# Optimization experiments

Measured on AMD Instinct MI355X. Metric: run time of the kernel, lower is better.

## Reference

```python
import jax, jax.numpy as jnp
import numpy as np

BLANK = 512            # blank_idx = vocab_size
DURATIONS = (1, 2, 3, 4)
SIGMA = 0.05           # logit under-normalization weight
NEG = -1e30            # safe -inf (keeps gradients finite)


def setup_inputs() -> dict:
    key = jax.random.key(0)
    k1, k2, k3 = jax.random.split(key, 3)
    B, T, U, V = 8, 256, 64, 512
    D = len(DURATIONS)
    label_acts = jax.random.normal(k1, (B, T, U + 1, V + 1), dtype=jnp.float32)
    duration_acts = jax.random.normal(k2, (B, T, U + 1, D), dtype=jnp.float32)
    targets = jax.random.randint(k3, (B, U), 0, V, dtype=jnp.int32)
    input_lengths = jnp.full((B,), T, dtype=jnp.int32)
    target_lengths = jnp.full((B,), U, dtype=jnp.int32)
    return {"label_acts": label_acts, "duration_acts": duration_acts,
            "targets": targets, "input_lengths": input_lengths,
            "target_lengths": target_lengths}


def _lag(x, d):
    # x: [T, ...] -> y with y[t] = x[t - d], NEG-padded at the front
    pad = jnp.full_like(x[:d], NEG)
    return jnp.concatenate([pad, x[: x.shape[0] - d]], axis=0)


def _tdt_loglike(label_acts, duration_acts, targets, input_lengths, target_lengths):
    B, T, U1, _ = label_acts.shape
    U = U1 - 1
    D = len(DURATIONS)

    lp = jax.nn.log_softmax(label_acts, axis=-1) - SIGMA        # [B,T,U+1,V+1]
    lpb = lp[..., BLANK]                                         # [B,T,U+1] blank logp
    lpy = jnp.take_along_axis(                                   # [B,T,U] target-label logp
        lp[:, :, :U, :], targets[:, None, :, None].astype(jnp.int32), axis=3
    )[..., 0]
    ld = jax.nn.log_softmax(duration_acts, axis=-1)              # [B,T,U+1,D]

    # time-major views for the scan
    lpb_t = jnp.transpose(lpb, (1, 0, 2))                        # [T,B,U+1]
    lpy_t = jnp.transpose(lpy, (1, 0, 2))                        # [T,B,U]
    ld_t = jnp.transpose(ld, (1, 0, 2, 3))                       # [T,B,U+1,D]

    # lagged emission terms: entry at scan step t is the value at t - duration
    lb_lag = jnp.stack([_lag(lpb_t, d) for d in DURATIONS], axis=1)                       # [T,D,B,U+1]
    ly_lag = jnp.stack([_lag(lpy_t, d) for d in DURATIONS], axis=1)                       # [T,D,B,U]
    ld_lag = jnp.stack([_lag(ld_t[..., i], d) for i, d in enumerate(DURATIONS)], axis=1)  # [T,D,B,U+1]

    dmax = max(DURATIONS)
    alpha0 = jnp.concatenate(
        [jnp.zeros((B, 1), jnp.float32), jnp.full((B, U), NEG, jnp.float32)], axis=1)     # [B,U+1]
    hist0 = jnp.concatenate(
        [alpha0[None], jnp.full((dmax - 1, B, U1), NEG, jnp.float32)], axis=0)            # [dmax,B,U+1]

    def step(hist, xs):
        # hist[a] = alpha[t-1-a]
        lb, ly, ldr = xs  # [D,B,U+1], [D,B,U], [D,B,U+1]
        blank_terms = jnp.stack([hist[d - 1] + lb[i] + ldr[i]
                                 for i, d in enumerate(DURATIONS)])      # [D,B,U+1]
        blank_in = jax.nn.logsumexp(blank_terms, axis=0)                 # [B,U+1]
        label_terms = jnp.stack([hist[d - 1][:, :U] + ly[i] + ldr[i][:, :U]
                                 for i, d in enumerate(DURATIONS)])      # [D,B,U]
        label_in = jax.nn.logsumexp(label_terms, axis=0)                 # [B,U]
        alpha_t = jnp.concatenate(
            [blank_in[:, :1], jnp.logaddexp(blank_in[:, 1:], label_in)], axis=1)
        hist = jnp.concatenate([alpha_t[None], hist[:-1]], axis=0)
        return hist, alpha_t

    _, alphas_rest = jax.lax.scan(step, hist0, (lb_lag[1:], ly_lag[1:], ld_lag[1:]))
    alphas = jnp.concatenate([alpha0[None], alphas_rest], axis=0)        # [T,B,U+1]

    # final: from (T_b - d, U_b) emit blank with duration d landing exactly at T_b
    dur = jnp.asarray(DURATIONS, jnp.int32)                              # [D]
    t_idx = input_lengths[:, None].astype(jnp.int32) - dur[None, :]      # [B,D]
    valid = t_idx >= 0
    t_safe = jnp.clip(t_idx, 0, T - 1)
    b_idx = jnp.arange(B)[:, None]
    u_idx = target_lengths[:, None].astype(jnp.int32)
    a_fin = alphas[t_safe, b_idx, u_idx]                                 # [B,D]
    lpb_fin = lpb[b_idx, t_safe, u_idx]                                  # [B,D]
    ld_fin = ld[b_idx, t_safe, u_idx, jnp.arange(D)[None, :]]            # [B,D]
    terms = jnp.where(valid, a_fin + lpb_fin + ld_fin, NEG)
    return jax.nn.logsumexp(terms, axis=1)                               # [B] log-likelihood


def reference(label_acts, duration_acts, targets, input_lengths, target_lengths):
    ll = _tdt_loglike(label_acts, duration_acts, targets, input_lengths, target_lengths)
    return jnp.mean(-ll)  # reduction='mean'
```

## Files before the change

### kernel.cpp

```cpp
#include <hip/hip_runtime.h>

#define TDT_B  8
#define TDT_T  256
#define TDT_U  64
#define TDT_U1 65
#define TDT_V1 513
#define TP     275
#define SIG    0.05f
#define SHIFT  3.0f

#define OFF_PYD 572000
#define OFF_GC  1135200

__global__ __launch_bounds__(256) void k_prep(
    const float* __restrict__ la, const float* __restrict__ da,
    const int* __restrict__ tgt, float* __restrict__ ws,
    float* __restrict__ out)
{
  if (blockIdx.x == 0 && threadIdx.x == 0) out[0] = 0.f;

  const int l = threadIdx.x & 63;
  const int r = (blockIdx.x << 2) + (threadIdx.x >> 6);
  const int u  = r % TDT_U1;
  const int bt = r / TDT_U1;
  const int t  = bt & (TDT_T - 1);
  const int b  = bt >> 8;

  const float* row = la + (size_t)r * TDT_V1;
  const int ofs = r & 1;
  const float2* p2 = (const float2*)(row + ofs);
  float2 w[4];
#pragma unroll
  for (int k = 0; k < 4; ++k) w[k] = p2[l + (k << 6)];
  const float extra = row[ofs ? 0 : 512];

  float m = extra;
#pragma unroll
  for (int k = 0; k < 4; ++k) m = fmaxf(m, fmaxf(w[k].x, w[k].y));
#pragma unroll
  for (int off = 32; off; off >>= 1) m = fmaxf(m, __shfl_xor(m, off));
  float s = (l == 0) ? __expf(extra - m) : 0.f;
#pragma unroll
  for (int k = 0; k < 4; ++k) s += __expf(w[k].x - m) + __expf(w[k].y - m);
#pragma unroll
  for (int off = 32; off; off >>= 1) s += __shfl_xor(s, off);
  const float lse = m + __logf(s);

  const float4 dv = *(const float4*)(da + ((size_t)r << 2));
  const float m4 = fmaxf(fmaxf(dv.x, dv.y), fmaxf(dv.z, dv.w));
  const float l4 = m4 + __logf(__expf(dv.x - m4) + __expf(dv.y - m4) +
                               __expf(dv.z - m4) + __expf(dv.w - m4));
  const float d0 = dv.x - l4 + SHIFT * 1.0f;
  const float d1 = dv.y - l4 + SHIFT * 2.0f;
  const float d2 = dv.z - l4 + SHIFT * 3.0f;
  const float d3 = dv.w - l4 + SHIFT * 4.0f;

  float4* WB4 = (float4*)ws;
  float4* WY4 = (float4*)(ws + OFF_PYD);
  float4* GC4 = (float4*)(ws + OFF_GC);

  const int tp = t + 4;
  const float xb = ofs ? w[3].y : extra;
  if (l == (ofs ? 63 : 0)) {
    const float pb = xb - lse - SIG;
    const float4 wb = make_float4(__expf(pb + d0), __expf(pb + d1),
                                  __expf(pb + d2), __expf(pb + d3));
    WB4[(b * TP + tp) * TDT_U1 + u] = wb;
    if (u == TDT_U) GC4[b * TP + tp] = wb;
  }

  const int tg = (u < TDT_U) ? tgt[b * TDT_U + u] : -1;
  bool own = false; float vt = 0.f;
#pragma unroll
  for (int k = 0; k < 4; ++k) {
    const int base = ofs + ((l + (k << 6)) << 1);
    if (base == tg)     { vt = w[k].x; own = true; }
    if (base + 1 == tg) { vt = w[k].y; own = true; }
  }
  if (ofs && tg == 0 && l == 0) { vt = extra; own = true; }
  if (own) {
    const float py = vt - lse - SIG;
    WY4[(b * TP + tp) * TDT_U + u] =
        make_float4(__expf(py + d0), __expf(py + d1), __expf(py + d2), __expf(py + d3));
  }

  if (t < 4 && l == 0) {
    const float4 z4 = make_float4(0.f, 0.f, 0.f, 0.f);
    WB4[(b * TP + t) * TDT_U1 + u] = z4;
    if (u == TDT_U) GC4[b * TP + t] = z4;
    if (u < TDT_U)  WY4[(b * TP + t) * TDT_U + u] = z4;
  }
}

__device__ __forceinline__ float shup1(float x) {
  const int r = __builtin_amdgcn_update_dpp(
      0, __float_as_int(x), 0x138, 0xf, 0xf, true);
  return __int_as_float(r);
}

__device__ __forceinline__ void gl2lds16(const float4* g, float4* lds) {
  __builtin_amdgcn_global_load_lds(
      (const __attribute__((address_space(1))) void*)g,
      (__attribute__((address_space(3))) void*)lds, 16, 0, 0);
}

__device__ __forceinline__ void fill_group(
    const float4* __restrict__ WB4p, const float4* __restrict__ WY4p,
    float4* ring, int j, int wv, int l)
{
  const int sb = 15 * j + wv;
  const int rb = 15 * (j % 3) + (wv - 1);
#pragma unroll
  for (int k = 0; k < 5; ++k) {
    const int s    = sb + 3 * k;
    const int slot = rb + 3 * k;
    gl2lds16(WB4p + (size_t)s * TDT_U1 + l, ring + slot * 128);
    gl2lds16(WY4p + (size_t)s * TDT_U  + l, ring + slot * 128 + 64);
  }
}

__global__ __launch_bounds__(256, 1) void k_dp(
    const float* __restrict__ ws, float* __restrict__ out)
{
  const int b  = blockIdx.x;
  const int wv = threadIdx.x >> 6;
  const int l  = threadIdx.x & 63;
  const float4* WB4p = (const float4*)ws + (size_t)b * (TP * TDT_U1);
  const float4* WY4p = (const float4*)(ws + OFF_PYD) + (size_t)b * (TP * TDT_U);
  const float4* GC4p = (const float4*)(ws + OFF_GC) + (size_t)b * TP;

  extern __shared__ float4 smem[];
  float4* ring = smem;
  float4* glds = smem + 45 * 128;

  if (wv != 0) {
    for (int i = (threadIdx.x - 64); i < TP; i += 192) glds[i] = GC4p[i];
    fill_group(WB4p, WY4p, ring, 0, wv, l);
    fill_group(WB4p, WY4p, ring, 1, wv, l);
  }
  __syncthreads();

  float4 B0,B1,B2,B3,B4,B5,B6,B7,B8,B9,B10,B11,B12,B13,B14;
  float4 Y0,Y1,Y2,Y3,Y4,Y5,Y6,Y7,Y8,Y9,Y10,Y11,Y12,Y13,Y14;
  float4 G0,G1,G2,G3,G4,G5,G6,G7,G8,G9,G10,G11,G12,G13,G14;
  float a1 = 0.f, a2 = 0.f, a3 = 0.f, a4 = 0.f;
  float c1 = 0.f, c2 = 0.f, c3 = 0.f, c4 = 0.f;
  float L = 0.f;

#define LOADSLOT(S, RS, TPI) do {            \
    const int _r = (RS) * 128;               \
    B##S = ring[_r + l];                     \
    Y##S = ring[_r + 64 + l];                \
    G##S = glds[TPI];                        \
  } while (0)

  if (wv == 0) {
    LOADSLOT(1, 0, 1);   LOADSLOT(2, 1, 2);   LOADSLOT(3, 2, 3);
    LOADSLOT(4, 3, 4);   LOADSLOT(5, 4, 5);   LOADSLOT(6, 5, 6);
    LOADSLOT(7, 6, 7);   LOADSLOT(8, 7, 8);   LOADSLOT(9, 8, 9);
    LOADSLOT(10, 9, 10); LOADSLOT(11, 10, 11);LOADSLOT(12, 11, 12);
    LOADSLOT(13, 12, 13);LOADSLOT(14, 13, 14);LOADSLOT(0, 14, 15);
    a1 = (l == 0) ? 1.f : 0.f;
  }

#define STEP(S0,S1,S2,S3, RSL, TPI) do {                                     \
    float ly0 = a1 * Y##S0.x, ly1 = a2 * Y##S1.y,                            \
          ly2 = a3 * Y##S2.z, ly3 = a4 * Y##S3.w;                            \
    float P  = (ly0 + ly1) + (ly2 + ly3);                                    \
    float m  = shup1(P);                                                     \
    float anew = ((a1*B##S0.x + a2*B##S1.y) + (a3*B##S2.z + a4*B##S3.w)) + m;\
    float cnew = ((c1*G##S0.x + c2*G##S1.y) + (c3*G##S2.z + c4*G##S3.w)) + P;\
    a4 = a3; a3 = a2; a2 = a1; a1 = anew;                                    \
    c4 = c3; c3 = c2; c2 = c1; c1 = cnew;                                    \
    LOADSLOT(S3, RSL, TPI);                                                  \
  } while (0)

  for (int i = 0, tb = 1; i < 17; ++i, tb += 15) {
    __syncthreads();
    if (wv != 0) {
      if (i < 16) fill_group(WB4p, WY4p, ring, i + 2, wv, l);
    } else {
      const int rbB = 15 * ((i + 1) % 3);
      if (i) {
        const float r1 = __shfl(a1, tb >> 3);
        const float r2 = __shfl(a1, tb >> 2);
        const float rl = fmaxf(r1, r2);
        const float sc = (rl > 1e-30f) ? (1.0f / rl) : 1.0f;
        L -= __logf(sc);
        a1 *= sc; a2 *= sc; a3 *= sc; a4 *= sc;
        c1 *= sc; c2 *= sc; c3 *= sc; c4 *= sc;
      }
      STEP(4,3,2,1,     rbB + 0,  tb + 15);
      STEP(5,4,3,2,     rbB + 1,  tb + 16);
      STEP(6,5,4,3,     rbB + 2,  tb + 17);
      STEP(7,6,5,4,     rbB + 3,  tb + 18);
      STEP(8,7,6,5,     rbB + 4,  tb + 19);
      STEP(9,8,7,6,     rbB + 5,  tb + 20);
      STEP(10,9,8,7,    rbB + 6,  tb + 21);
      STEP(11,10,9,8,   rbB + 7,  tb + 22);
      STEP(12,11,10,9,  rbB + 8,  tb + 23);
      STEP(13,12,11,10, rbB + 9,  tb + 24);
      STEP(14,13,12,11, rbB + 10, tb + 25);
      STEP(0,14,13,12,  rbB + 11, tb + 26);
      STEP(1,0,14,13,   rbB + 12, tb + 27);
      STEP(2,1,0,14,    rbB + 13, tb + 28);
      STEP(3,2,1,0,     rbB + 14, tb + 29);
    }
  }

  if (wv == 0 && l == 63) {
    const float sum = c1 * glds[259].x
                    + c2 * glds[258].y
                    + c3 * glds[257].z
                    + c4 * glds[256].w;
    const float ll = L - SHIFT * 256.0f + __logf(sum);
    atomicAdd(out, ll * (-1.0f / TDT_B));
  }
#undef STEP
#undef LOADSLOT
}

extern "C" void kernel_launch(void* const* d_in, const int* in_sizes, int n_in,
                              void* d_out, int out_size, void* d_ws, size_t ws_size,
                              hipStream_t stream)
{
  const float* la = (const float*)d_in[0];
  const float* da = (const float*)d_in[1];
  const int*   tg = (const int*)d_in[2];
  float* ws  = (float*)d_ws;
  float* out = (float*)d_out;

  const int rows = TDT_B * TDT_T * TDT_U1;
  k_prep<<<rows / 4, 256, 0, stream>>>(la, da, tg, ws, out);
  k_dp  <<<TDT_B, 256, (45 * 128 + TP) * sizeof(float4), stream>>>(ws, out);
}
```

Before: 78.63 us.

## Collapse DP kernel to a single wave with async LDS prefetch and no barriers

The DP kernel now runs one 64-lane wave per batch instead of one compute wave plus three loader waves. That wave issues its own global-to-LDS prefetches one group ahead and uses s_waitcnt on outstanding vector-memory loads instead of __syncthreads. The rescale step now uses readlane instead of shfl, and the recurrence is rewritten with explicit FMAs. This removes block-wide barriers and cross-wave handoff from the serial critical path. The cost is that load issue and waiting now sit in the compute wave's own instruction stream, and correctness depends on the hand-written vmcnt counts and the in-order completion they assume.

```diff
diff --git a/kernel.cpp b/kernel.cpp
--- a/kernel.cpp
+++ b/kernel.cpp
@@ -98,33 +98,21 @@
   return __int_as_float(r);
 }
 
+__device__ __forceinline__ float rdlane(float x, int lane) {
+  return __int_as_float(__builtin_amdgcn_readlane(__float_as_int(x), lane));
+}
+
 __device__ __forceinline__ void gl2lds16(const float4* g, float4* lds) {
   __builtin_amdgcn_global_load_lds(
       (const __attribute__((address_space(1))) void*)g,
       (__attribute__((address_space(3))) void*)lds, 16, 0, 0);
 }
 
-__device__ __forceinline__ void fill_group(
-    const float4* __restrict__ WB4p, const float4* __restrict__ WY4p,
-    float4* ring, int j, int wv, int l)
-{
-  const int sb = 15 * j + wv;
-  const int rb = 15 * (j % 3) + (wv - 1);
-#pragma unroll
-  for (int k = 0; k < 5; ++k) {
-    const int s    = sb + 3 * k;
-    const int slot = rb + 3 * k;
-    gl2lds16(WB4p + (size_t)s * TDT_U1 + l, ring + slot * 128);
-    gl2lds16(WY4p + (size_t)s * TDT_U  + l, ring + slot * 128 + 64);
-  }
-}
-
-__global__ __launch_bounds__(256, 1) void k_dp(
+__global__ __launch_bounds__(64, 1) void k_dp(
     const float* __restrict__ ws, float* __restrict__ out)
 {
-  const int b  = blockIdx.x;
-  const int wv = threadIdx.x >> 6;
-  const int l  = threadIdx.x & 63;
+  const int b = blockIdx.x;
+  const int l = threadIdx.x;
   const float4* WB4p = (const float4*)ws + (size_t)b * (TP * TDT_U1);
   const float4* WY4p = (const float4*)(ws + OFF_PYD) + (size_t)b * (TP * TDT_U);
   const float4* GC4p = (const float4*)(ws + OFF_GC) + (size_t)b * TP;
@@ -133,19 +121,19 @@
   float4* ring = smem;
   float4* glds = smem + 45 * 128;
 
-  if (wv != 0) {
-    for (int i = (threadIdx.x - 64); i < TP; i += 192) glds[i] = GC4p[i];
-    fill_group(WB4p, WY4p, ring, 0, wv, l);
-    fill_group(WB4p, WY4p, ring, 1, wv, l);
-  }
-  __syncthreads();
+#pragma unroll
+  for (int k = 0; k < 5; ++k) gl2lds16(GC4p + k * 64 + l, glds + k * 64);
+#pragma unroll
+  for (int s = 1; s <= 30; ++s) {
+    gl2lds16(WB4p + (size_t)s * TDT_U1 + l, ring + (s - 1) * 128);
+    gl2lds16(WY4p + (size_t)s * TDT_U  + l, ring + (s - 1) * 128 + 64);
+  }
+  asm volatile("s_waitcnt vmcnt(0)" ::: "memory");
+  __builtin_amdgcn_sched_barrier(0);
 
   float4 B0,B1,B2,B3,B4,B5,B6,B7,B8,B9,B10,B11,B12,B13,B14;
   float4 Y0,Y1,Y2,Y3,Y4,Y5,Y6,Y7,Y8,Y9,Y10,Y11,Y12,Y13,Y14;
   float4 G0,G1,G2,G3,G4,G5,G6,G7,G8,G9,G10,G11,G12,G13,G14;
-  float a1 = 0.f, a2 = 0.f, a3 = 0.f, a4 = 0.f;
-  float c1 = 0.f, c2 = 0.f, c3 = 0.f, c4 = 0.f;
-  float L = 0.f;
 
 #define LOADSLOT(S, RS, TPI) do {            \
     const int _r = (RS) * 128;               \
@@ -154,42 +142,58 @@
     G##S = glds[TPI];                        \
   } while (0)
 
-  if (wv == 0) {
-    LOADSLOT(1, 0, 1);   LOADSLOT(2, 1, 2);   LOADSLOT(3, 2, 3);
-    LOADSLOT(4, 3, 4);   LOADSLOT(5, 4, 5);   LOADSLOT(6, 5, 6);
-    LOADSLOT(7, 6, 7);   LOADSLOT(8, 7, 8);   LOADSLOT(9, 8, 9);
-    LOADSLOT(10, 9, 10); LOADSLOT(11, 10, 11);LOADSLOT(12, 11, 12);
-    LOADSLOT(13, 12, 13);LOADSLOT(14, 13, 14);LOADSLOT(0, 14, 15);
-    a1 = (l == 0) ? 1.f : 0.f;
-  }
+  LOADSLOT(1, 0, 1);   LOADSLOT(2, 1, 2);   LOADSLOT(3, 2, 3);
+  LOADSLOT(4, 3, 4);   LOADSLOT(5, 4, 5);   LOADSLOT(6, 5, 6);
+  LOADSLOT(7, 6, 7);   LOADSLOT(8, 7, 8);   LOADSLOT(9, 8, 9);
+  LOADSLOT(10, 9, 10); LOADSLOT(11, 10, 11);LOADSLOT(12, 11, 12);
+  LOADSLOT(13, 12, 13);LOADSLOT(14, 13, 14);LOADSLOT(0, 14, 15);
+
+  float a1 = (l == 0) ? 1.f : 0.f, a2 = 0.f, a3 = 0.f, a4 = 0.f;
+  float c1 = 0.f, c2 = 0.f, c3 = 0.f, c4 = 0.f;
+  float L = 0.f;
 
 #define STEP(S0,S1,S2,S3, RSL, TPI) do {                                     \
-    float ly0 = a1 * Y##S0.x, ly1 = a2 * Y##S1.y,                            \
-          ly2 = a3 * Y##S2.z, ly3 = a4 * Y##S3.w;                            \
-    float P  = (ly0 + ly1) + (ly2 + ly3);                                    \
-    float m  = shup1(P);                                                     \
-    float anew = ((a1*B##S0.x + a2*B##S1.y) + (a3*B##S2.z + a4*B##S3.w)) + m;\
-    float cnew = ((c1*G##S0.x + c2*G##S1.y) + (c3*G##S2.z + c4*G##S3.w)) + P;\
+    float p01 = fmaf(a2, Y##S1.y, a1 * Y##S0.x);                             \
+    float p23 = fmaf(a4, Y##S3.w, a3 * Y##S2.z);                             \
+    float P   = p01 + p23;                                                   \
+    float m   = shup1(P);                                                    \
+    float b01 = fmaf(a2, B##S1.y, a1 * B##S0.x);                             \
+    float b23 = fmaf(a4, B##S3.w, a3 * B##S2.z);                             \
+    float q01 = fmaf(c2, G##S1.y, c1 * G##S0.x);                             \
+    float q23 = fmaf(c4, G##S3.w, c3 * G##S2.z);                             \
+    float anew = (b01 + b23) + m;                                            \
+    float cnew = (q01 + q23) + P;                                            \
     a4 = a3; a3 = a2; a2 = a1; a1 = anew;                                    \
     c4 = c3; c3 = c2; c2 = c1; c1 = cnew;                                    \
     LOADSLOT(S3, RSL, TPI);                                                  \
   } while (0)
 
   for (int i = 0, tb = 1; i < 17; ++i, tb += 15) {
-    __syncthreads();
-    if (wv != 0) {
-      if (i < 16) fill_group(WB4p, WY4p, ring, i + 2, wv, l);
+    if (i <= 15) {
+      const int sb = 15 * (i + 2) + 1;
+      const int rb = (15 * (i + 2)) % 45;
+#pragma unroll
+      for (int k = 0; k < 15; ++k) {
+        gl2lds16(WB4p + (size_t)(sb + k) * TDT_U1 + l, ring + (rb + k) * 128);
+        gl2lds16(WY4p + (size_t)(sb + k) * TDT_U  + l, ring + (rb + k) * 128 + 64);
+      }
+      asm volatile("s_waitcnt vmcnt(30)" ::: "memory");
     } else {
-      const int rbB = 15 * ((i + 1) % 3);
-      if (i) {
-        const float r1 = __shfl(a1, tb >> 3);
-        const float r2 = __shfl(a1, tb >> 2);
-        const float rl = fmaxf(r1, r2);
-        const float sc = (rl > 1e-30f) ? (1.0f / rl) : 1.0f;
-        L -= __logf(sc);
-        a1 *= sc; a2 *= sc; a3 *= sc; a4 *= sc;
-        c1 *= sc; c2 *= sc; c3 *= sc; c4 *= sc;
-      }
+      asm volatile("s_waitcnt vmcnt(0)" ::: "memory");
+    }
+    __builtin_amdgcn_sched_barrier(0);
+
+    if (i) {
+      const float r1 = rdlane(a1, tb >> 3);
+      const float r2 = rdlane(a1, tb >> 2);
+      const float rl = fmaxf(r1, r2);
+      const float sc = (rl > 1e-30f) ? (1.0f / rl) : 1.0f;
+      L -= __logf(sc);
+      a1 *= sc; a2 *= sc; a3 *= sc; a4 *= sc;
+      c1 *= sc; c2 *= sc; c3 *= sc; c4 *= sc;
+    }
+    {
+      const int rbB = (15 * (i + 1)) % 45;
       STEP(4,3,2,1,     rbB + 0,  tb + 15);
       STEP(5,4,3,2,     rbB + 1,  tb + 16);
       STEP(6,5,4,3,     rbB + 2,  tb + 17);
@@ -208,7 +212,7 @@
     }
   }
 
-  if (wv == 0 && l == 63) {
+  if (l == 63) {
     const float sum = c1 * glds[259].x
                     + c2 * glds[258].y
                     + c3 * glds[257].z
@@ -232,5 +236,5 @@
 
   const int rows = TDT_B * TDT_T * TDT_U1;
   k_prep<<<rows / 4, 256, 0, stream>>>(la, da, tg, ws, out);
-  k_dp  <<<TDT_B, 256, (45 * 128 + TP) * sizeof(float4), stream>>>(ws, out);
-}
+  k_dp  <<<TDT_B, 64, (45 * 128 + 320) * sizeof(float4), stream>>>(ws, out);
+}
```

New measurement: 92.67 us. 1.18x slower.

## Replace syncthreads with raw barrier and partial vmcnt waits in DP loop

Applied to the files above, without the earlier changes.

Changes the per-group synchronisation in the DP kernel. Producer waves now wait only for the older group's async global-to-LDS loads (vmcnt(10)) before hitting a raw s_barrier, so the newest group can stay in flight instead of being drained by __syncthreads. The consumer wave uses s_barrier directly, switches the rescale shuffles to readlane, and rewrites the step arithmetic as FMA chains to shorten the dependency path. The risk is getting the manual vmcnt accounting wrong, which could let the consumer read ring slots that have not finished loading.

```diff
diff --git a/kernel.cpp b/kernel.cpp
--- a/kernel.cpp
+++ b/kernel.cpp
@@ -98,6 +98,10 @@
   return __int_as_float(r);
 }
 
+__device__ __forceinline__ float rdlane(float x, int lane) {
+  return __int_as_float(__builtin_amdgcn_readlane(__float_as_int(x), lane));
+}
+
 __device__ __forceinline__ void gl2lds16(const float4* g, float4* lds) {
   __builtin_amdgcn_global_load_lds(
       (const __attribute__((address_space(1))) void*)g,
@@ -164,32 +168,45 @@
   }
 
 #define STEP(S0,S1,S2,S3, RSL, TPI) do {                                     \
-    float ly0 = a1 * Y##S0.x, ly1 = a2 * Y##S1.y,                            \
-          ly2 = a3 * Y##S2.z, ly3 = a4 * Y##S3.w;                            \
-    float P  = (ly0 + ly1) + (ly2 + ly3);                                    \
-    float m  = shup1(P);                                                     \
-    float anew = ((a1*B##S0.x + a2*B##S1.y) + (a3*B##S2.z + a4*B##S3.w)) + m;\
-    float cnew = ((c1*G##S0.x + c2*G##S1.y) + (c3*G##S2.z + c4*G##S3.w)) + P;\
+    float p01 = fmaf(a2, Y##S1.y, a1 * Y##S0.x);                             \
+    float p23 = fmaf(a4, Y##S3.w, a3 * Y##S2.z);                             \
+    float P   = p01 + p23;                                                   \
+    float m   = shup1(P);                                                    \
+    float b01 = fmaf(a2, B##S1.y, a1 * B##S0.x);                             \
+    float b23 = fmaf(a4, B##S3.w, a3 * B##S2.z);                             \
+    float q01 = fmaf(c2, G##S1.y, c1 * G##S0.x);                             \
+    float q23 = fmaf(c4, G##S3.w, c3 * G##S2.z);                             \
+    float anew = (b01 + b23) + m;                                            \
+    float cnew = (q01 + q23) + P;                                            \
     a4 = a3; a3 = a2; a2 = a1; a1 = anew;                                    \
     c4 = c3; c3 = c2; c2 = c1; c1 = cnew;                                    \
     LOADSLOT(S3, RSL, TPI);                                                  \
   } while (0)
 
   for (int i = 0, tb = 1; i < 17; ++i, tb += 15) {
-    __syncthreads();
     if (wv != 0) {
-      if (i < 16) fill_group(WB4p, WY4p, ring, i + 2, wv, l);
+      if (i <= 15) {
+        fill_group(WB4p, WY4p, ring, i + 2, wv, l);
+        asm volatile("s_waitcnt vmcnt(10)" ::: "memory");
+      } else {
+        asm volatile("s_waitcnt vmcnt(0)" ::: "memory");
+      }
+      __builtin_amdgcn_sched_barrier(0);
+      __builtin_amdgcn_s_barrier();
     } else {
-      const int rbB = 15 * ((i + 1) % 3);
+      __builtin_amdgcn_sched_barrier(0);
+      __builtin_amdgcn_s_barrier();
+      __builtin_amdgcn_sched_barrier(0);
       if (i) {
-        const float r1 = __shfl(a1, tb >> 3);
-        const float r2 = __shfl(a1, tb >> 2);
+        const float r1 = rdlane(a1, tb >> 3);
+        const float r2 = rdlane(a1, tb >> 2);
         const float rl = fmaxf(r1, r2);
         const float sc = (rl > 1e-30f) ? (1.0f / rl) : 1.0f;
         L -= __logf(sc);
         a1 *= sc; a2 *= sc; a3 *= sc; a4 *= sc;
         c1 *= sc; c2 *= sc; c3 *= sc; c4 *= sc;
       }
+      const int rbB = 15 * ((i + 1) % 3);
       STEP(4,3,2,1,     rbB + 0,  tb + 15);
       STEP(5,4,3,2,     rbB + 1,  tb + 16);
       STEP(6,5,4,3,     rbB + 2,  tb + 17);
```

After: 77.52 us (median of 2 runs). No clear change (-1.4%).
